# Optimization experiments

Measured on AMD Instinct MI355X. Metric: run time of the kernel, lower is better.

## Reference

```python
import jax, jax.numpy as jnp
import numpy as np

N, P, K, LF = 1024, 20000, 8, 1  # samples, in_features(=fold_num at stride 1), kernel_size, local_feature


def setup_inputs() -> dict:
    key = jax.random.key(0)
    k1, k2 = jax.random.split(key)
    X = jax.random.normal(k1, (N, P), dtype=jnp.float32)
    # GlorotUniform over weight tensor (fold_num, kernel_size, local_feature)
    limit = np.sqrt(6.0 / (K + LF)).astype(np.float32)
    W = jax.random.uniform(k2, (P, K, LF), dtype=jnp.float32, minval=-limit, maxval=limit)
    b = jnp.zeros((P, LF), dtype=jnp.float32)
    return {"X": X, "W": W, "b": b}


def reference(X, W, b):
    # Pad right by kernel_size-1 (same as tf.pad with [[0,0],[0,K-1]])
    Xp = jnp.pad(X, ((0, 0), (0, K - 1)))  # [N, P+K-1]
    # im2col: sliding windows of length K at stride 1 -> [N, P, K]
    idx = jnp.arange(P)[:, None] + jnp.arange(K)[None, :]  # [P, K]
    patches = Xp[:, idx]  # [N, P, K]
    # per-position matmul with distinct weights W[p] in R^{KxLF}, LF=1
    AL = jnp.einsum('npk,pkl->npl', patches, W) + b  # [N, P, 1]
    return AL.reshape(X.shape[0], P)  # [N, P]
```

## Files before the change

kernel.cpp:

```cpp
#include <hip/hip_runtime.h>


constexpr int N  = 1024;
constexpr int P  = 20000;
constexpr int K  = 8;
constexpr int P4 = P / 4;
constexpr int COLS_PADDED = 5120;
constexpr int NCHUNKS = 64;
constexpr int ROWS = N / NCHUNKS;

__global__ __launch_bounds__(256)
void local_linear_kernel(const float* __restrict__ X,
                         const float* __restrict__ W,
                         const float* __restrict__ b,
                         float* __restrict__ out) {
    int tid   = blockIdx.x * blockDim.x + threadIdx.x;
    int chunk = tid / COLS_PADDED;
    int q     = tid - chunk * COLS_PADDED;
    if (q >= P4) return;

    int p  = q * 4;
    int n0 = chunk * ROWS;

    const float* wp = W + (size_t)p * K;
    float wv[32];
    #pragma unroll
    for (int i = 0; i < 8; ++i) {
        float4 w4 = *reinterpret_cast<const float4*>(wp + i * 4);
        wv[i * 4 + 0] = w4.x;
        wv[i * 4 + 1] = w4.y;
        wv[i * 4 + 2] = w4.z;
        wv[i * 4 + 3] = w4.w;
    }
    float4 bv = *reinterpret_cast<const float4*>(b + p);

    const bool interior = (p + 12 <= P);

    for (int r = 0; r < ROWS; ++r) {
        const float* xrow = X + (size_t)(n0 + r) * P;

        float xv[12];
        if (interior) {
            float4 a = *reinterpret_cast<const float4*>(xrow + p);
            float4 c = *reinterpret_cast<const float4*>(xrow + p + 4);
            float4 d = *reinterpret_cast<const float4*>(xrow + p + 8);
            xv[0] = a.x; xv[1] = a.y; xv[2]  = a.z; xv[3]  = a.w;
            xv[4] = c.x; xv[5] = c.y; xv[6]  = c.z; xv[7]  = c.w;
            xv[8] = d.x; xv[9] = d.y; xv[10] = d.z; xv[11] = d.w;
        } else {
            #pragma unroll
            for (int i = 0; i < 12; ++i)
                xv[i] = (p + i < P) ? xrow[p + i] : 0.0f;
        }

        float r0 = bv.x, r1 = bv.y, r2 = bv.z, r3 = bv.w;
        #pragma unroll
        for (int k = 0; k < K; ++k) {
            r0 += xv[0 + k] * wv[0  + k];
            r1 += xv[1 + k] * wv[8  + k];
            r2 += xv[2 + k] * wv[16 + k];
            r3 += xv[3 + k] * wv[24 + k];
        }

        float4 o; o.x = r0; o.y = r1; o.z = r2; o.w = r3;
        *reinterpret_cast<float4*>(out + (size_t)(n0 + r) * P + p) = o;
    }
}

extern "C" void kernel_launch(void* const* d_in, const int* in_sizes, int n_in,
                              void* d_out, int out_size, void* d_ws, size_t ws_size,
                              hipStream_t stream) {
    const float* X = (const float*)d_in[0];
    const float* W = (const float*)d_in[1];
    const float* b = (const float*)d_in[2];
    float* out = (float*)d_out;

    constexpr int total_threads = COLS_PADDED * NCHUNKS;
    constexpr int block = 256;
    constexpr int grid = total_threads / block;

    local_linear_kernel<<<grid, block, 0, stream>>>(X, W, b, out);
}
```

Baseline: 35.14 us.

## Transpose weights, double row chunks, unroll rows, use nontemporal output stores

Adds a pre-pass kernel that transposes W into a k-major workspace so each thread loads its weights as coalesced float4s. The main kernel now splits rows into twice as many chunks for more parallelism, unrolls the row loop, sets an occupancy hint in launch bounds, and writes output with nontemporal stores to avoid polluting cache. The extra kernel launch and workspace traffic add fixed overhead. The kernel is bandwidth bound, so the benefit of these changes is uncertain.

New measurement: 37.01 us. 1.05x slower.

```diff
diff --git a/kernel.cpp b/kernel.cpp
--- a/kernel.cpp
+++ b/kernel.cpp
@@ -6,36 +6,44 @@
 constexpr int K  = 8;
 constexpr int P4 = P / 4;
 constexpr int COLS_PADDED = 5120;
-constexpr int NCHUNKS = 64;
+constexpr int NCHUNKS = 128;
 constexpr int ROWS = N / NCHUNKS;
 
+typedef float float4n __attribute__((ext_vector_type(4)));
+
 __global__ __launch_bounds__(256)
+void transpose_w(const float* __restrict__ W, float* __restrict__ Wt) {
+    int p = blockIdx.x * blockDim.x + threadIdx.x;
+    if (p >= P) return;
+    float4 a = *reinterpret_cast<const float4*>(W + (size_t)p * K);
+    float4 c = *reinterpret_cast<const float4*>(W + (size_t)p * K + 4);
+    Wt[0 * P + p] = a.x; Wt[1 * P + p] = a.y;
+    Wt[2 * P + p] = a.z; Wt[3 * P + p] = a.w;
+    Wt[4 * P + p] = c.x; Wt[5 * P + p] = c.y;
+    Wt[6 * P + p] = c.z; Wt[7 * P + p] = c.w;
+}
+
+__global__ __launch_bounds__(256, 4)
 void local_linear_kernel(const float* __restrict__ X,
-                         const float* __restrict__ W,
+                         const float* __restrict__ Wt,
                          const float* __restrict__ b,
                          float* __restrict__ out) {
-    int tid   = blockIdx.x * blockDim.x + threadIdx.x;
-    int chunk = tid / COLS_PADDED;
-    int q     = tid - chunk * COLS_PADDED;
+    const int tid   = blockIdx.x * blockDim.x + threadIdx.x;
+    const int chunk = tid / COLS_PADDED;
+    const int q     = tid - chunk * COLS_PADDED;
     if (q >= P4) return;
+    const int p  = q * 4;
+    const int n0 = chunk * ROWS;
 
-    int p  = q * 4;
-    int n0 = chunk * ROWS;
-
-    const float* wp = W + (size_t)p * K;
-    float wv[32];
+    float4 wv[8];
     #pragma unroll
-    for (int i = 0; i < 8; ++i) {
-        float4 w4 = *reinterpret_cast<const float4*>(wp + i * 4);
-        wv[i * 4 + 0] = w4.x;
-        wv[i * 4 + 1] = w4.y;
-        wv[i * 4 + 2] = w4.z;
-        wv[i * 4 + 3] = w4.w;
-    }
-    float4 bv = *reinterpret_cast<const float4*>(b + p);
+    for (int k = 0; k < K; ++k)
+        wv[k] = *reinterpret_cast<const float4*>(Wt + (size_t)k * P + p);
+    const float4 bv = *reinterpret_cast<const float4*>(b + p);
 
     const bool interior = (p + 12 <= P);
 
+    #pragma unroll 4
     for (int r = 0; r < ROWS; ++r) {
         const float* xrow = X + (size_t)(n0 + r) * P;
 
@@ -56,14 +64,15 @@
         float r0 = bv.x, r1 = bv.y, r2 = bv.z, r3 = bv.w;
         #pragma unroll
         for (int k = 0; k < K; ++k) {
-            r0 += xv[0 + k] * wv[0  + k];
-            r1 += xv[1 + k] * wv[8  + k];
-            r2 += xv[2 + k] * wv[16 + k];
-            r3 += xv[3 + k] * wv[24 + k];
+            r0 += xv[k + 0] * wv[k].x;
+            r1 += xv[k + 1] * wv[k].y;
+            r2 += xv[k + 2] * wv[k].z;
+            r3 += xv[k + 3] * wv[k].w;
         }
 
-        float4 o; o.x = r0; o.y = r1; o.z = r2; o.w = r3;
-        *reinterpret_cast<float4*>(out + (size_t)(n0 + r) * P + p) = o;
+        float4n o; o.x = r0; o.y = r1; o.z = r2; o.w = r3;
+        __builtin_nontemporal_store(
+            o, reinterpret_cast<float4n*>(out + (size_t)(n0 + r) * P + p));
     }
 }
 
@@ -79,5 +88,7 @@
     constexpr int block = 256;
     constexpr int grid = total_threads / block;
 
-    local_linear_kernel<<<grid, block, 0, stream>>>(X, W, b, out);
+    float* Wt = (float*)d_ws;
+    transpose_w<<<(P + block - 1) / block, block, 0, stream>>>(W, Wt);
+    local_linear_kernel<<<grid, block, 0, stream>>>(X, Wt, b, out);
 }
```
